# Optimization experiments

Hardware: AMD Instinct MI355X
Metric: run time of the kernel (lower is better)

## Reference

```python
import jax, jax.numpy as jnp
import numpy as np

N_CLUSTERS = 8
N_DIMS = 4
N_POINTS = 2_000_000


def setup_inputs() -> dict:
    key = jax.random.key(0)
    k1, k2, k3, k4 = jax.random.split(key, 4)
    return {
        "X": jax.random.normal(k1, (N_POINTS, N_DIMS), dtype=jnp.float32),
        "means": jax.random.normal(k2, (N_CLUSTERS, N_DIMS), dtype=jnp.float32),
        "chols": jax.random.normal(k3, (N_CLUSTERS, N_DIMS, N_DIMS), dtype=jnp.float32),
        "weights": jax.random.normal(k4, (N_CLUSTERS,), dtype=jnp.float32),
        "it": 0,
    }


def reference(X, means, chols, weights, it):
    N, D = X.shape
    K = means.shape[0]
    # sigmas[k] = tril(L_k) @ tril(L_k)^T + I  (cholesky_comp)
    L = jnp.tril(chols)                                   # [K,D,D]
    sigmas = L @ jnp.swapaxes(L, -1, -2) + jnp.eye(D, dtype=X.dtype)
    S_inv = jnp.linalg.inv(sigmas)                        # [K,D,D]
    dets = jnp.linalg.det(sigmas)                         # [K]
    two_pi_D = (2.0 * jnp.pi) ** D
    # per-cluster Gaussian densities over all points: dens[k,n]
    diff = X[None, :, :] - means[:, None, :]              # [K,N,D]
    mahal = jnp.einsum('knd,kde,kne->kn', diff, S_inv, diff)  # [K,N]
    dens = jnp.exp(-0.5 * mahal) / jnp.sqrt(two_pi_D * dets)[:, None]
    # pairwise softmax weights over all K^2 (i,j) products w_i*w_j
    wij = weights[:, None] * weights[None, :]             # [K,K]
    W = jax.nn.softmax(wij.reshape(-1)).reshape(K, K)
    # squared-mixture normaliser: z = sum_ij W_ij * N(mu_i; mu_j, S_i+S_j)
    Ssum = sigmas[:, None] + sigmas[None, :]              # [K,K,D,D]
    det_sum = jnp.linalg.det(Ssum)                        # [K,K]
    mdiff = means[:, None, :] - means[None, :, :]         # [K,K,D]
    md = jnp.einsum('ijd,ijde,ije->ij', mdiff, jnp.linalg.inv(Ssum), mdiff)
    norm_term = jnp.exp(-0.5 * md) / jnp.sqrt(two_pi_D * det_sum)
    z = jnp.sum(W * norm_term)
    # numerator: sum_ij W_ij dens_i dens_j  (factored to avoid [K^2,N])
    num = jnp.einsum('in,jn,ij->n', dens, dens, W)        # [N]
    pdf = num / z
    # forward: -(logsumexp over points of log pdf) / N
    out = -(jax.scipy.special.logsumexp(jnp.log(pdf)) / N)
    return out
```

## Files before the change

### kernel.cpp

```cpp
#include <hip/hip_runtime.h>
#include <math.h>


struct WsLayout {
  double P[36][32];
  double Wp[36];
  double logz;
  float a2[8][10];
  float bb[8][4];
  float cc[8];
};

__device__ inline void chol4(const double S[4][4], double G[4][4]) {
  #pragma unroll
  for (int i = 0; i < 4; ++i) {
    #pragma unroll
    for (int j = 0; j < 4; ++j) {
      if (j > i) { G[i][j] = 0.0; continue; }
      double s = S[i][j];
      #pragma unroll
      for (int m = 0; m < 4; ++m) if (m < j) s -= G[i][m] * G[j][m];
      if (i == j) G[i][j] = sqrt(s);
      else        G[i][j] = s / G[j][j];
    }
  }
}

__global__ void prep_kernel(const float* __restrict__ means,
                            const float* __restrict__ chols,
                            const float* __restrict__ weights,
                            WsLayout* ws) {
  __shared__ double sig[8][4][4];
  const double LOG2E = 1.4426950408889634074;
  const double LN2PI = 1.8378770664093454836;
  const int t = threadIdx.x;

  if (t < 8) {
    const int k = t;
    double L[4][4], S[4][4];
    #pragma unroll
    for (int i = 0; i < 4; ++i)
      #pragma unroll
      for (int j = 0; j < 4; ++j)
        L[i][j] = (j <= i) ? (double)chols[k * 16 + i * 4 + j] : 0.0;
    #pragma unroll
    for (int i = 0; i < 4; ++i)
      #pragma unroll
      for (int j = 0; j < 4; ++j) {
        double s = (i == j) ? 1.0 : 0.0;
        #pragma unroll
        for (int m = 0; m < 4; ++m) s += L[i][m] * L[j][m];
        S[i][j] = s;
        sig[k][i][j] = s;
      }
    double G[4][4];
    chol4(S, G);
    const double logdet =
        2.0 * (log(G[0][0]) + log(G[1][1]) + log(G[2][2]) + log(G[3][3]));
    double Gi[4][4];
    #pragma unroll
    for (int j = 0; j < 4; ++j) {
      #pragma unroll
      for (int i = 0; i < 4; ++i) {
        if (i < j) { Gi[i][j] = 0.0; continue; }
        double s = (i == j) ? 1.0 : 0.0;
        #pragma unroll
        for (int m = 0; m < 4; ++m)
          if (m >= j && m < i) s -= G[i][m] * Gi[m][j];
        Gi[i][j] = s / G[i][i];
      }
    }
    double A[4][4];
    #pragma unroll
    for (int i = 0; i < 4; ++i)
      #pragma unroll
      for (int j = 0; j < 4; ++j) {
        double s = 0.0;
        #pragma unroll
        for (int m = 0; m < 4; ++m) s += Gi[m][i] * Gi[m][j];
        A[i][j] = s;
      }
    double mu[4];
    #pragma unroll
    for (int i = 0; i < 4; ++i) mu[i] = (double)means[k * 4 + i];
    double bmu[4];
    #pragma unroll
    for (int i = 0; i < 4; ++i) {
      double s = 0.0;
      #pragma unroll
      for (int j = 0; j < 4; ++j) s += A[i][j] * mu[j];
      bmu[i] = s;
    }
    double muAmu = 0.0;
    #pragma unroll
    for (int i = 0; i < 4; ++i) muAmu += mu[i] * bmu[i];
    const double logcoef = -0.5 * (4.0 * LN2PI + logdet);
    int tt = 0;
    #pragma unroll
    for (int i = 0; i < 4; ++i)
      #pragma unroll
      for (int j = i; j < 4; ++j, ++tt)
        ws->a2[k][tt] =
            (float)(-0.5 * LOG2E * A[i][j] * ((i == j) ? 1.0 : 2.0));
    #pragma unroll
    for (int i = 0; i < 4; ++i) ws->bb[k][i] = (float)(LOG2E * bmu[i]);
    ws->cc[k] = (float)(LOG2E * (logcoef - 0.5 * muAmu));
  }
  __syncthreads();

  const int i = t >> 3, j = t & 7;
  const double wij = (double)weights[i] * (double)weights[j];
  double m = wij;
  #pragma unroll
  for (int o = 32; o > 0; o >>= 1) {
    double x = __shfl_xor(m, o, 64);
    m = fmax(m, x);
  }
  const double e = exp(wij - m);
  double ssum = e;
  #pragma unroll
  for (int o = 32; o > 0; o >>= 1) ssum += __shfl_xor(ssum, o, 64);
  const double Wij = e / ssum;

  double SS[4][4];
  #pragma unroll
  for (int a = 0; a < 4; ++a)
    #pragma unroll
    for (int b = 0; b < 4; ++b) SS[a][b] = sig[i][a][b] + sig[j][a][b];
  double G2[4][4];
  chol4(SS, G2);
  const double logdetS =
      2.0 * (log(G2[0][0]) + log(G2[1][1]) + log(G2[2][2]) + log(G2[3][3]));
  double bvec[4], y[4];
  #pragma unroll
  for (int a = 0; a < 4; ++a)
    bvec[a] = (double)means[i * 4 + a] - (double)means[j * 4 + a];
  #pragma unroll
  for (int a = 0; a < 4; ++a) {
    double s = bvec[a];
    #pragma unroll
    for (int mm = 0; mm < 4; ++mm) if (mm < a) s -= G2[a][mm] * y[mm];
    y[a] = s / G2[a][a];
  }
  const double md = y[0]*y[0] + y[1]*y[1] + y[2]*y[2] + y[3]*y[3];
  double zterm = Wij * exp(-0.5 * md - 0.5 * (4.0 * LN2PI + logdetS));
  #pragma unroll
  for (int o = 32; o > 0; o >>= 1) zterm += __shfl_xor(zterm, o, 64);
  if (t == 0) ws->logz = log(zterm);

  if (i <= j) {
    const int u = 8 * i - (i * (i - 1)) / 2 + (j - i);
    ws->Wp[u] = Wij * ((i == j) ? 1.0 : 2.0);
  }
  double* Pf = &ws->P[0][0];
  for (int u = t; u < 36 * 32; u += 64) Pf[u] = 0.0;
}

__global__ __launch_bounds__(256, 4) void point_kernel(
    const float4* __restrict__ X, const float* __restrict__ par,
    double* __restrict__ accg, int n) {
  float a2[8][10], bb[8][4], cc[8];
  #pragma unroll
  for (int k = 0; k < 8; ++k) {
    #pragma unroll
    for (int u = 0; u < 10; ++u) a2[k][u] = par[k * 10 + u];
    #pragma unroll
    for (int u = 0; u < 4; ++u) bb[k][u] = par[80 + k * 4 + u];
    cc[k] = par[112 + k];
  }
  float acc[36];
  #pragma unroll
  for (int u = 0; u < 36; ++u) acc[u] = 0.0f;

  const int S = gridDim.x * blockDim.x;
  const int idx = blockIdx.x * blockDim.x + threadIdx.x;
  for (int base = idx; base < n; base += 4 * S) {
    float4 v[4];
    float kill[4];
    #pragma unroll
    for (int j = 0; j < 4; ++j) {
      const int ij = base + j * S;
      const bool ok = ij < n;
      kill[j] = ok ? 0.0f : -1.0e30f;
      v[j] = X[ok ? ij : 0];
    }
    #pragma unroll
    for (int j = 0; j < 4; ++j) {
      const float4 vv = v[j];
      const float p[10] = {vv.x * vv.x, vv.x * vv.y, vv.x * vv.z, vv.x * vv.w,
                           vv.y * vv.y, vv.y * vv.z, vv.y * vv.w,
                           vv.z * vv.z, vv.z * vv.w, vv.w * vv.w};
      float d[8];
      #pragma unroll
      for (int k = 0; k < 8; ++k) {
        float a = cc[k] + kill[j];
        #pragma unroll
        for (int u = 0; u < 10; ++u) a = fmaf(a2[k][u], p[u], a);
        a = fmaf(bb[k][0], vv.x, a);
        a = fmaf(bb[k][1], vv.y, a);
        a = fmaf(bb[k][2], vv.z, a);
        a = fmaf(bb[k][3], vv.w, a);
        d[k] = __builtin_amdgcn_exp2f(a);
      }
      int u = 0;
      #pragma unroll
      for (int a_ = 0; a_ < 8; ++a_)
        #pragma unroll
        for (int b_ = a_; b_ < 8; ++b_, ++u)
          acc[u] = fmaf(d[a_], d[b_], acc[u]);
    }
  }

  const int lane = threadIdx.x & 63;
  const int wid = threadIdx.x >> 6;
  __shared__ float lred[4][36];
  #pragma unroll
  for (int u = 0; u < 36; ++u) {
    float vv = acc[u];
    #pragma unroll
    for (int o = 32; o > 0; o >>= 1) vv += __shfl_xor(vv, o, 64);
    if (lane == 0) lred[wid][u] = vv;
  }
  __syncthreads();
  if (threadIdx.x < 36) {
    const double s = (double)lred[0][threadIdx.x] + (double)lred[1][threadIdx.x] +
                     (double)lred[2][threadIdx.x] + (double)lred[3][threadIdx.x];
    unsafeAtomicAdd(&accg[threadIdx.x * 32 + (blockIdx.x & 31)], s);
  }
}

__global__ void final_kernel(const WsLayout* __restrict__ ws,
                             float* __restrict__ out, int n) {
  const int t = threadIdx.x;
  double val = 0.0;
  if (t < 36) {
    double s = 0.0;
    #pragma unroll
    for (int b = 0; b < 32; ++b) s += ws->P[t][b];
    val = ws->Wp[t] * s;
  }
  #pragma unroll
  for (int o = 32; o > 0; o >>= 1) val += __shfl_xor(val, o, 64);
  if (t == 0) out[0] = (float)(-(log(val) - ws->logz) / (double)n);
}

extern "C" void kernel_launch(void* const* d_in, const int* in_sizes, int n_in,
                              void* d_out, int out_size, void* d_ws, size_t ws_size,
                              hipStream_t stream) {
  const float* X       = (const float*)d_in[0];
  const float* means   = (const float*)d_in[1];
  const float* chols   = (const float*)d_in[2];
  const float* weights = (const float*)d_in[3];
  const int npoints = in_sizes[0] / 4;

  WsLayout* ws = (WsLayout*)d_ws;
  prep_kernel<<<1, 64, 0, stream>>>(means, chols, weights, ws);
  point_kernel<<<2048, 256, 0, stream>>>((const float4*)X, &ws->a2[0][0],
                                         &ws->P[0][0], npoints);
  final_kernel<<<1, 64, 0, stream>>>(ws, (float*)d_out, npoints);
}
```

Before: 111.4 us.

## Fold prep into point and final kernels, drop atomics, factor quadratic form

Removes the separate prep kernel. Each point-kernel block now recomputes the per-cluster quadratic parameters in shared memory while its first X loads are in flight, and the pairwise normaliser moves into the final kernel. Global double atomics are replaced by per-block partial writes that a 256-thread final kernel reduces. The quadratic form is evaluated Horner-style with wave-uniform parameters. This saves one launch and the atomic traffic, at the cost of redundant per-block double-precision setup and a larger final reduction.

```diff
diff --git a/kernel.cpp b/kernel.cpp
--- a/kernel.cpp
+++ b/kernel.cpp
@@ -2,14 +2,7 @@
 #include <math.h>
 
 
-struct WsLayout {
-  double P[36][32];
-  double Wp[36];
-  double logz;
-  float a2[8][10];
-  float bb[8][4];
-  float cc[8];
-};
+#define NBLK 2048
 
 __device__ inline void chol4(const double S[4][4], double G[4][4]) {
   #pragma unroll
@@ -26,18 +19,33 @@
   }
 }
 
-__global__ void prep_kernel(const float* __restrict__ means,
-                            const float* __restrict__ chols,
-                            const float* __restrict__ weights,
-                            WsLayout* ws) {
-  __shared__ double sig[8][4][4];
-  const double LOG2E = 1.4426950408889634074;
-  const double LN2PI = 1.8378770664093454836;
+__device__ __forceinline__ float uniformf(float x) {
+  return __int_as_float(__builtin_amdgcn_readfirstlane(__float_as_int(x)));
+}
+
+__global__ __launch_bounds__(256, 4) void point_kernel(
+    const float4* __restrict__ X, const float* __restrict__ means,
+    const float* __restrict__ chols, double* __restrict__ partial, int n) {
+  __shared__ float pp[8][16];
   const int t = threadIdx.x;
+  const int S = gridDim.x * blockDim.x;
+  const int idx = blockIdx.x * blockDim.x + t;
+
+  float4 v[4];
+  float kill[4];
+  #pragma unroll
+  for (int j = 0; j < 4; ++j) {
+    const int ij = idx + j * S;
+    const bool ok = ij < n;
+    kill[j] = ok ? 0.0f : -1.0e30f;
+    v[j] = X[ok ? ij : 0];
+  }
 
   if (t < 8) {
+    const double LOG2E = 1.4426950408889634074;
+    const double LN2PI = 1.8378770664093454836;
     const int k = t;
-    double L[4][4], S[4][4];
+    double L[4][4], Sm[4][4];
     #pragma unroll
     for (int i = 0; i < 4; ++i)
       #pragma unroll
@@ -50,11 +58,10 @@
         double s = (i == j) ? 1.0 : 0.0;
         #pragma unroll
         for (int m = 0; m < 4; ++m) s += L[i][m] * L[j][m];
-        S[i][j] = s;
-        sig[k][i][j] = s;
+        Sm[i][j] = s;
       }
     double G[4][4];
-    chol4(S, G);
+    chol4(Sm, G);
     const double logdet =
         2.0 * (log(G[0][0]) + log(G[1][1]) + log(G[2][2]) + log(G[3][3]));
     double Gi[4][4];
@@ -100,119 +107,71 @@
     for (int i = 0; i < 4; ++i)
       #pragma unroll
       for (int j = i; j < 4; ++j, ++tt)
-        ws->a2[k][tt] =
-            (float)(-0.5 * LOG2E * A[i][j] * ((i == j) ? 1.0 : 2.0));
-    #pragma unroll
-    for (int i = 0; i < 4; ++i) ws->bb[k][i] = (float)(LOG2E * bmu[i]);
-    ws->cc[k] = (float)(LOG2E * (logcoef - 0.5 * muAmu));
+        pp[k][tt] = (float)(-0.5 * LOG2E * A[i][j] * ((i == j) ? 1.0 : 2.0));
+    #pragma unroll
+    for (int i = 0; i < 4; ++i) pp[k][10 + i] = (float)(LOG2E * bmu[i]);
+    pp[k][14] = (float)(LOG2E * (logcoef - 0.5 * muAmu));
+    pp[k][15] = 0.0f;
   }
   __syncthreads();
 
-  const int i = t >> 3, j = t & 7;
-  const double wij = (double)weights[i] * (double)weights[j];
-  double m = wij;
-  #pragma unroll
-  for (int o = 32; o > 0; o >>= 1) {
-    double x = __shfl_xor(m, o, 64);
-    m = fmax(m, x);
-  }
-  const double e = exp(wij - m);
-  double ssum = e;
-  #pragma unroll
-  for (int o = 32; o > 0; o >>= 1) ssum += __shfl_xor(ssum, o, 64);
-  const double Wij = e / ssum;
-
-  double SS[4][4];
-  #pragma unroll
-  for (int a = 0; a < 4; ++a)
-    #pragma unroll
-    for (int b = 0; b < 4; ++b) SS[a][b] = sig[i][a][b] + sig[j][a][b];
-  double G2[4][4];
-  chol4(SS, G2);
-  const double logdetS =
-      2.0 * (log(G2[0][0]) + log(G2[1][1]) + log(G2[2][2]) + log(G2[3][3]));
-  double bvec[4], y[4];
-  #pragma unroll
-  for (int a = 0; a < 4; ++a)
-    bvec[a] = (double)means[i * 4 + a] - (double)means[j * 4 + a];
-  #pragma unroll
-  for (int a = 0; a < 4; ++a) {
-    double s = bvec[a];
-    #pragma unroll
-    for (int mm = 0; mm < 4; ++mm) if (mm < a) s -= G2[a][mm] * y[mm];
-    y[a] = s / G2[a][a];
-  }
-  const double md = y[0]*y[0] + y[1]*y[1] + y[2]*y[2] + y[3]*y[3];
-  double zterm = Wij * exp(-0.5 * md - 0.5 * (4.0 * LN2PI + logdetS));
-  #pragma unroll
-  for (int o = 32; o > 0; o >>= 1) zterm += __shfl_xor(zterm, o, 64);
-  if (t == 0) ws->logz = log(zterm);
-
-  if (i <= j) {
-    const int u = 8 * i - (i * (i - 1)) / 2 + (j - i);
-    ws->Wp[u] = Wij * ((i == j) ? 1.0 : 2.0);
-  }
-  double* Pf = &ws->P[0][0];
-  for (int u = t; u < 36 * 32; u += 64) Pf[u] = 0.0;
-}
-
-__global__ __launch_bounds__(256, 4) void point_kernel(
-    const float4* __restrict__ X, const float* __restrict__ par,
-    double* __restrict__ accg, int n) {
-  float a2[8][10], bb[8][4], cc[8];
-  #pragma unroll
-  for (int k = 0; k < 8; ++k) {
-    #pragma unroll
-    for (int u = 0; u < 10; ++u) a2[k][u] = par[k * 10 + u];
-    #pragma unroll
-    for (int u = 0; u < 4; ++u) bb[k][u] = par[80 + k * 4 + u];
-    cc[k] = par[112 + k];
-  }
+  float par[8][15];
+  #pragma unroll
+  for (int k = 0; k < 8; ++k)
+    #pragma unroll
+    for (int u = 0; u < 15; ++u) par[k][u] = uniformf(pp[k][u]);
+
   float acc[36];
   #pragma unroll
   for (int u = 0; u < 36; ++u) acc[u] = 0.0f;
 
-  const int S = gridDim.x * blockDim.x;
-  const int idx = blockIdx.x * blockDim.x + threadIdx.x;
   for (int base = idx; base < n; base += 4 * S) {
-    float4 v[4];
-    float kill[4];
+    if (base != idx) {
+      #pragma unroll
+      for (int j = 0; j < 4; ++j) {
+        const int ij = base + j * S;
+        const bool ok = ij < n;
+        kill[j] = ok ? 0.0f : -1.0e30f;
+        v[j] = X[ok ? ij : 0];
+      }
+    }
+    float d[4][8];
+    #pragma unroll
+    for (int k = 0; k < 8; ++k) {
+      #pragma unroll
+      for (int j = 0; j < 4; ++j) {
+        const float4 vv = v[j];
+        float t0 = fmaf(par[k][0], vv.x, par[k][10]);
+        t0 = fmaf(par[k][1], vv.y, t0);
+        t0 = fmaf(par[k][2], vv.z, t0);
+        t0 = fmaf(par[k][3], vv.w, t0);
+        float t1 = fmaf(par[k][4], vv.y, par[k][11]);
+        t1 = fmaf(par[k][5], vv.z, t1);
+        t1 = fmaf(par[k][6], vv.w, t1);
+        float t2 = fmaf(par[k][7], vv.z, par[k][12]);
+        t2 = fmaf(par[k][8], vv.w, t2);
+        float t3 = fmaf(par[k][9], vv.w, par[k][13]);
+        float a = par[k][14] + kill[j];
+        a = fmaf(vv.x, t0, a);
+        a = fmaf(vv.y, t1, a);
+        a = fmaf(vv.z, t2, a);
+        a = fmaf(vv.w, t3, a);
+        d[j][k] = __builtin_amdgcn_exp2f(a);
+      }
+    }
     #pragma unroll
     for (int j = 0; j < 4; ++j) {
-      const int ij = base + j * S;
-      const bool ok = ij < n;
-      kill[j] = ok ? 0.0f : -1.0e30f;
-      v[j] = X[ok ? ij : 0];
-    }
-    #pragma unroll
-    for (int j = 0; j < 4; ++j) {
-      const float4 vv = v[j];
-      const float p[10] = {vv.x * vv.x, vv.x * vv.y, vv.x * vv.z, vv.x * vv.w,
-                           vv.y * vv.y, vv.y * vv.z, vv.y * vv.w,
-                           vv.z * vv.z, vv.z * vv.w, vv.w * vv.w};
-      float d[8];
-      #pragma unroll
-      for (int k = 0; k < 8; ++k) {
-        float a = cc[k] + kill[j];
-        #pragma unroll
-        for (int u = 0; u < 10; ++u) a = fmaf(a2[k][u], p[u], a);
-        a = fmaf(bb[k][0], vv.x, a);
-        a = fmaf(bb[k][1], vv.y, a);
-        a = fmaf(bb[k][2], vv.z, a);
-        a = fmaf(bb[k][3], vv.w, a);
-        d[k] = __builtin_amdgcn_exp2f(a);
-      }
       int u = 0;
       #pragma unroll
       for (int a_ = 0; a_ < 8; ++a_)
         #pragma unroll
         for (int b_ = a_; b_ < 8; ++b_, ++u)
-          acc[u] = fmaf(d[a_], d[b_], acc[u]);
-    }
-  }
-
-  const int lane = threadIdx.x & 63;
-  const int wid = threadIdx.x >> 6;
+          acc[u] = fmaf(d[j][a_], d[j][b_], acc[u]);
+    }
+  }
+
+  const int lane = t & 63;
+  const int wid = t >> 6;
   __shared__ float lred[4][36];
   #pragma unroll
   for (int u = 0; u < 36; ++u) {
@@ -222,26 +181,119 @@
     if (lane == 0) lred[wid][u] = vv;
   }
   __syncthreads();
-  if (threadIdx.x < 36) {
-    const double s = (double)lred[0][threadIdx.x] + (double)lred[1][threadIdx.x] +
-                     (double)lred[2][threadIdx.x] + (double)lred[3][threadIdx.x];
-    unsafeAtomicAdd(&accg[threadIdx.x * 32 + (blockIdx.x & 31)], s);
-  }
-}
-
-__global__ void final_kernel(const WsLayout* __restrict__ ws,
+  if (t < 36) {
+    const double s = (double)lred[0][t] + (double)lred[1][t] +
+                     (double)lred[2][t] + (double)lred[3][t];
+    partial[t * NBLK + blockIdx.x] = s;
+  }
+}
+
+__global__ void final_kernel(const double* __restrict__ partial,
+                             const float* __restrict__ means,
+                             const float* __restrict__ chols,
+                             const float* __restrict__ weights,
                              float* __restrict__ out, int n) {
+  const double LN2PI = 1.8378770664093454836;
   const int t = threadIdx.x;
-  double val = 0.0;
-  if (t < 36) {
-    double s = 0.0;
-    #pragma unroll
-    for (int b = 0; b < 32; ++b) s += ws->P[t][b];
-    val = ws->Wp[t] * s;
-  }
-  #pragma unroll
-  for (int o = 32; o > 0; o >>= 1) val += __shfl_xor(val, o, 64);
-  if (t == 0) out[0] = (float)(-(log(val) - ws->logz) / (double)n);
+  __shared__ double sig[8][4][4];
+  __shared__ double red[4][36];
+  __shared__ double Wp[36];
+  __shared__ double logz_s;
+
+  if (t < 8) {
+    const int k = t;
+    double L[4][4];
+    #pragma unroll
+    for (int i = 0; i < 4; ++i)
+      #pragma unroll
+      for (int j = 0; j < 4; ++j)
+        L[i][j] = (j <= i) ? (double)chols[k * 16 + i * 4 + j] : 0.0;
+    #pragma unroll
+    for (int i = 0; i < 4; ++i)
+      #pragma unroll
+      for (int j = 0; j < 4; ++j) {
+        double s = (i == j) ? 1.0 : 0.0;
+        #pragma unroll
+        for (int m = 0; m < 4; ++m) s += L[i][m] * L[j][m];
+        sig[k][i][j] = s;
+      }
+  }
+
+  double a36[36];
+  #pragma unroll
+  for (int u = 0; u < 36; ++u) a36[u] = 0.0;
+  for (int b = t; b < NBLK; b += 256) {
+    #pragma unroll
+    for (int u = 0; u < 36; ++u) a36[u] += partial[u * NBLK + b];
+  }
+  __syncthreads();
+
+  const int lane = t & 63;
+  const int wid = t >> 6;
+  #pragma unroll
+  for (int u = 0; u < 36; ++u) {
+    double vv = a36[u];
+    #pragma unroll
+    for (int o = 32; o > 0; o >>= 1) vv += __shfl_xor(vv, o, 64);
+    if (lane == 0) red[wid][u] = vv;
+  }
+
+  if (t < 64) {
+    const int i = t >> 3, j = t & 7;
+    const double wij = (double)weights[i] * (double)weights[j];
+    double m = wij;
+    #pragma unroll
+    for (int o = 32; o > 0; o >>= 1) {
+      double x = __shfl_xor(m, o, 64);
+      m = fmax(m, x);
+    }
+    const double e = exp(wij - m);
+    double ssum = e;
+    #pragma unroll
+    for (int o = 32; o > 0; o >>= 1) ssum += __shfl_xor(ssum, o, 64);
+    const double Wij = e / ssum;
+
+    double SS[4][4];
+    #pragma unroll
+    for (int a = 0; a < 4; ++a)
+      #pragma unroll
+      for (int b = 0; b < 4; ++b) SS[a][b] = sig[i][a][b] + sig[j][a][b];
+    double G2[4][4];
+    chol4(SS, G2);
+    const double logdetS =
+        2.0 * (log(G2[0][0]) + log(G2[1][1]) + log(G2[2][2]) + log(G2[3][3]));
+    double bvec[4], y[4];
+    #pragma unroll
+    for (int a = 0; a < 4; ++a)
+      bvec[a] = (double)means[i * 4 + a] - (double)means[j * 4 + a];
+    #pragma unroll
+    for (int a = 0; a < 4; ++a) {
+      double s = bvec[a];
+      #pragma unroll
+      for (int mm = 0; mm < 4; ++mm) if (mm < a) s -= G2[a][mm] * y[mm];
+      y[a] = s / G2[a][a];
+    }
+    const double md = y[0]*y[0] + y[1]*y[1] + y[2]*y[2] + y[3]*y[3];
+    double zterm = Wij * exp(-0.5 * md - 0.5 * (4.0 * LN2PI + logdetS));
+    #pragma unroll
+    for (int o = 32; o > 0; o >>= 1) zterm += __shfl_xor(zterm, o, 64);
+    if (t == 0) logz_s = log(zterm);
+
+    if (i <= j) {
+      const int u = 8 * i - (i * (i - 1)) / 2 + (j - i);
+      Wp[u] = Wij * ((i == j) ? 1.0 : 2.0);
+    }
+  }
+  __syncthreads();
+
+  if (t < 64) {
+    double val = 0.0;
+    if (t < 36)
+      val = Wp[t] * (red[0][t] + red[1][t] + red[2][t] + red[3][t]);
+    #pragma unroll
+    for (int o = 32; o > 0; o >>= 1) val += __shfl_xor(val, o, 64);
+    if (t == 0) out[0] = (float)(-(log(val) - logz_s) / (double)n);
+  }
 }
 
 extern "C" void kernel_launch(void* const* d_in, const int* in_sizes, int n_in,
@@ -253,9 +305,9 @@
   const float* weights = (const float*)d_in[3];
   const int npoints = in_sizes[0] / 4;
 
-  WsLayout* ws = (WsLayout*)d_ws;
-  prep_kernel<<<1, 64, 0, stream>>>(means, chols, weights, ws);
-  point_kernel<<<2048, 256, 0, stream>>>((const float4*)X, &ws->a2[0][0],
-                                         &ws->P[0][0], npoints);
-  final_kernel<<<1, 64, 0, stream>>>(ws, (float*)d_out, npoints);
-}
+  double* partial = (double*)d_ws;
+  point_kernel<<<NBLK, 256, 0, stream>>>((const float4*)X, means, chols,
+                                         partial, npoints);
+  final_kernel<<<1, 256, 0, stream>>>(partial, means, chols, weights,
+                                      (float*)d_out, npoints);
+}
```

Result: slower. 146.3 us (+31.4%).
